# Kernel optimization log

Measured on AMD Instinct MI355X. Metric: run time of the kernel, lower is better.

The kernel has to match this reference:

```python
import jax, jax.numpy as jnp
import numpy as np

SEGMENT_LENGTHS = (2048, 4096, 8192)
DILATION_RATES = (1, 2, 4)
NUM_HEADS = 12
EMBED_DIM = 768
B, N = 2, 8192


def setup_inputs() -> dict:
    key = jax.random.key(0)
    ks = jax.random.split(key, 11)
    E = EMBED_DIM
    return {
        "query": jax.random.normal(ks[0], (B, N, E), jnp.float32),
        "key": jax.random.normal(ks[1], (B, N, E), jnp.float32),
        "value": jax.random.normal(ks[2], (B, N, E), jnp.float32),
        "Wq": jax.random.normal(ks[3], (E, E), jnp.float32) * (E ** -0.5),
        "bq": jax.random.normal(ks[4], (E,), jnp.float32) * 0.02,
        "Wk": jax.random.normal(ks[5], (E, E), jnp.float32) * (E ** -0.5),
        "bk": jax.random.normal(ks[6], (E,), jnp.float32) * 0.02,
        "Wv": jax.random.normal(ks[7], (E, E), jnp.float32) * (E ** -0.5),
        "bv": jax.random.normal(ks[8], (E,), jnp.float32) * 0.02,
        "Wo": jax.random.normal(ks[9], (E, E), jnp.float32) * (E ** -0.5),
        "bo": jax.random.normal(ks[10], (E,), jnp.float32) * 0.02,
    }


def _dilated_attention(q, k, v):
    # q, k, v: [b, n, h, d]
    b, n, h, d = q.shape
    num_groups = len(DILATION_RATES)
    g = h // num_groups  # heads per dilation group
    scale = float(1.0 / np.sqrt(d))  # xformers default softmax scale
    out = jnp.zeros_like(q)
    for i, (r, s) in enumerate(zip(DILATION_RATES, SEGMENT_LENGTHS)):
        off = i % r
        hmin, hmax = i * g, (i + 1) * g
        nseg = n // s
        # gather: [b, nseg, s/r, g, d]
        qg = q.reshape(b, nseg, s, h, d)[:, :, off::r, hmin:hmax, :]
        kg = k.reshape(b, nseg, s, h, d)[:, :, off::r, hmin:hmax, :]
        vg = v.reshape(b, nseg, s, h, d)[:, :, off::r, hmin:hmax, :]
        scores = jnp.einsum("bnqhd,bnkhd->bnhqk", qg, kg) * scale
        attn = jax.nn.softmax(scores, axis=-1)
        x = jnp.einsum("bnhqk,bnkhd->bnqhd", attn, vg)
        out = (
            out.reshape(b, nseg, s, h, d)
            .at[:, :, off::r, hmin:hmax, :]
            .add(x)
            .reshape(b, n, h, d)
        )
    # faithful to original: normalize by sum over the sequence dimension
    return out / jnp.sum(out, axis=1, keepdims=True)


def reference(query, key, value, Wq, bq, Wk, bk, Wv, bv, Wo, bo):
    b, n, e = query.shape
    h = NUM_HEADS
    d = e // h
    q = (query @ Wq.T + bq).reshape(b, n, h, d)
    k = (key @ Wk.T + bk).reshape(b, n, h, d)
    v = (value @ Wv.T + bv).reshape(b, n, h, d)
    x = _dilated_attention(q, k, v)
    x = x.reshape(b, n, e)
    return x @ Wo.T + bo
```

## Files before the change

kernel.cpp:

```cpp
#include <hip/hip_runtime.h>
#include <hip/hip_bf16.h>
#include <cmath>
#include <cstdint>

#define B_ 2
#define N_ 8192
#define H_ 12
#define D_ 64
#define E_ 768
#define M_ (B_*N_)

typedef __attribute__((ext_vector_type(8))) short short8;
typedef __attribute__((ext_vector_type(4))) short short4v;
typedef __attribute__((ext_vector_type(4))) float float4v;
typedef __attribute__((ext_vector_type(2))) unsigned uint2v;

__device__ inline short f2b(float f) {
  union { float f; unsigned u; } x; x.f = f;
  unsigned r = (x.u + 0x7fffu + ((x.u >> 16) & 1u)) >> 16;
  return (short)r;
}
__device__ inline float b2f(short s) {
  union { unsigned u; float f; } x; x.u = ((unsigned)(unsigned short)s) << 16;
  return x.f;
}
__device__ inline void split2(float f, short& h, short& l) {
  h = f2b(f);
  l = f2b(f - b2f(h));
}
__device__ inline void split_rn1(float f, unsigned& hi16, float& lo) {
  unsigned u = __float_as_uint(f);
  unsigned r = u + 0x7fffu + ((u >> 16) & 1u);
  hi16 = r >> 16;
  lo = f - __uint_as_float(hi16 << 16);
}
__device__ inline unsigned pack_trunc(float a, float b) {
  return (__float_as_uint(b) & 0xffff0000u) | (__float_as_uint(a) >> 16);
}

#define MFMA(a, b, c) __builtin_amdgcn_mfma_f32_16x16x32_bf16((a), (b), (c), 0, 0, 0)

#define GLOAD_LDS16(g, l) \
  __builtin_amdgcn_global_load_lds((const __attribute__((address_space(1))) void*)(g), \
      (__attribute__((address_space(3))) void*)(l), 16, 0, 0)

__global__ __launch_bounds__(256) void split_kernel(const float* __restrict__ src,
    short* __restrict__ hi, short* __restrict__ lo, int count4)
{
  int i = blockIdx.x * 256 + threadIdx.x;
  if (i >= count4) return;
  float4v t = ((const float4v*)src)[i];
  short4v h4, l4; short hh, ll;
  split2(t.x, hh, ll); h4.x = hh; l4.x = ll;
  split2(t.y, hh, ll); h4.y = hh; l4.y = ll;
  split2(t.z, hh, ll); h4.z = hh; l4.z = ll;
  split2(t.w, hh, ll); h4.w = hh; l4.w = ll;
  ((short4v*)hi)[i] = h4;
  ((short4v*)lo)[i] = l4;
}

__global__ __launch_bounds__(256) void inv_kernel(const float* __restrict__ sums,
    float* __restrict__ inv)
{
  int i = blockIdx.x * 256 + threadIdx.x;
  if (i < B_ * E_) inv[i] = 1.0f / sums[i];
}

template<int AMODE, bool OUT_PAIR>
__global__ __launch_bounds__(256) void gemm_xwT(const float* __restrict__ Ap,
    const float* __restrict__ inv, const short* __restrict__ Wh,
    const short* __restrict__ Wl, const float* __restrict__ bias,
    void* __restrict__ OutH, short* __restrict__ OutL)
{
  __shared__ short Ash[128 * 40], Asl[128 * 40];
  __shared__ short Wsh[128 * 32], Wsl[128 * 32];
  const int tid = threadIdx.x;
  const int m0 = blockIdx.y * 128;
  const int n0 = blockIdx.x * 128;
  const int w = tid >> 6, lane = tid & 63, quad = lane >> 4, l16 = lane & 15;
  const int wr = w >> 1, wc = w & 1;
  const int cq = (l16 >> 1) & 3;

  float4v acc[4][4];
#pragma unroll
  for (int a = 0; a < 4; ++a)
#pragma unroll
    for (int c = 0; c < 4; ++c) acc[a][c] = (float4v)0.0f;

  for (int kt = 0; kt < 24; ++kt) {
    const int k0 = kt * 32;
#pragma unroll
    for (int i = 0; i < 2; ++i) {
      int slot = w * 128 + i * 64 + lane;
      int row = slot >> 2, cs = slot & 3;
      int cl = cs ^ ((row >> 1) & 3);
      size_t go = (size_t)(n0 + row) * E_ + k0 + cl * 8;
      GLOAD_LDS16(Wh + go, &Wsh[slot * 8]);
      GLOAD_LDS16(Wl + go, &Wsl[slot * 8]);
    }
#pragma unroll
    for (int p = 0; p < 4; ++p) {
      int idx = tid + p * 256;
      int row = idx >> 3, c4 = (idx & 7) * 4;
      float4v t = *(const float4v*)(Ap + (size_t)(m0 + row) * E_ + k0 + c4);
      if constexpr (AMODE == 1) {
        float4v iv = *(const float4v*)(inv + (m0 >> 13) * E_ + k0 + c4);
        t *= iv;
      }
      unsigned h0, h1, h2, h3; float l0, l1, l2, l3;
      split_rn1(t.x, h0, l0); split_rn1(t.y, h1, l1);
      split_rn1(t.z, h2, l2); split_rn1(t.w, h3, l3);
      uint2v hp, lp;
      hp.x = h0 | (h1 << 16); hp.y = h2 | (h3 << 16);
      lp.x = pack_trunc(l0, l1); lp.y = pack_trunc(l2, l3);
      *(uint2v*)&Ash[row * 40 + c4] = hp;
      *(uint2v*)&Asl[row * 40 + c4] = lp;
    }
    __syncthreads();

    short8 afh[4], afl[4], bfh[4], bfl[4];
#pragma unroll
    for (int rt = 0; rt < 4; ++rt) {
      afh[rt] = *(const short8*)&Ash[(wr * 64 + rt * 16 + l16) * 40 + quad * 8];
      afl[rt] = *(const short8*)&Asl[(wr * 64 + rt * 16 + l16) * 40 + quad * 8];
    }
#pragma unroll
    for (int ct = 0; ct < 4; ++ct) {
      int wrow = (wc * 64 + ct * 16 + l16) * 32 + (quad ^ cq) * 8;
      bfh[ct] = *(const short8*)&Wsh[wrow];
      bfl[ct] = *(const short8*)&Wsl[wrow];
    }
#pragma unroll
    for (int rt = 0; rt < 4; ++rt)
#pragma unroll
      for (int ct = 0; ct < 4; ++ct) {
        float4v a = acc[rt][ct];
        a = MFMA(afh[rt], bfh[ct], a);
        a = MFMA(afh[rt], bfl[ct], a);
        a = MFMA(afl[rt], bfh[ct], a);
        acc[rt][ct] = a;
      }
    __syncthreads();
  }

#pragma unroll
  for (int ct = 0; ct < 4; ++ct) {
    int n = n0 + wc * 64 + ct * 16 + l16;
    float bv = bias[n];
#pragma unroll
    for (int rt = 0; rt < 4; ++rt) {
#pragma unroll
      for (int i = 0; i < 4; ++i) {
        int m = m0 + wr * 64 + rt * 16 + quad * 4 + i;
        float v = acc[rt][ct][i] + bv;
        if constexpr (OUT_PAIR) {
          short hh, ll; split2(v, hh, ll);
          ((short*)OutH)[(size_t)m * E_ + n] = hh;
          OutL[(size_t)m * E_ + n] = ll;
        } else {
          ((float*)OutH)[(size_t)m * E_ + n] = v;
        }
      }
    }
  }
}

__device__ __host__ inline int hoff_of(int g, int hg) {
  return g == 0 ? hg * 8192 : (g == 1 ? 32768 + hg * 4096 : 49152 + hg * 2048);
}

__global__ __launch_bounds__(256) void transpose_v(const short* __restrict__ vh,
    const short* __restrict__ vl, short* __restrict__ vgh, short* __restrict__ vgl)
{
  __shared__ short Lh[64 * 68], Ll[64 * 68];
  int bid = blockIdx.x;
  int b = 0;
  if (bid >= 896) { b = 1; bid -= 896; }
  int g, hg, tile;
  if (bid < 512)      { g = 0; hg = bid >> 7; tile = bid & 127; }
  else if (bid < 768) { g = 1; hg = (bid - 512) >> 6; tile = (bid - 512) & 63; }
  else                { g = 2; hg = (bid - 768) >> 5; tile = (bid - 768) & 31; }
  const int h = g * 4 + hg, r = 1 << g, off = g;
  const int ext = 8192 >> g;
  const int jj0 = tile * 64, seg = jj0 >> 11, j0 = jj0 & 2047;
  const int n0 = seg * (2048 << g) + off + j0 * r;
  const int tid = threadIdx.x;

#pragma unroll
  for (int p = 0; p < 2; ++p) {
    int c = tid + p * 256;
    int jr = c >> 3, c8 = (c & 7) * 8;
    size_t gsrc = ((size_t)(b * N_ + n0 + jr * r) * H_ + h) * D_ + c8;
    *(short8*)&Lh[jr * 68 + c8] = *(const short8*)(vh + gsrc);
    *(short8*)&Ll[jr * 68 + c8] = *(const short8*)(vl + gsrc);
  }
  __syncthreads();
  size_t basebh = ((size_t)b * 57344 + hoff_of(g, hg)) * 64;
#pragma unroll
  for (int p = 0; p < 2; ++p) {
    int c = tid + p * 256;
    int dd = c >> 3, jc = (c & 7) * 8;
    short8 oh, ol;
#pragma unroll
    for (int u = 0; u < 8; ++u) {
      oh[u] = Lh[(jc + u) * 68 + dd];
      ol[u] = Ll[(jc + u) * 68 + dd];
    }
    size_t gdst = basebh + (size_t)dd * ext + jj0 + jc;
    *(short8*)(vgh + gdst) = oh;
    *(short8*)(vgl + gdst) = ol;
  }
}

__global__ __launch_bounds__(256) void attn_kernel(
    const short* __restrict__ qh, const short* __restrict__ ql,
    const short* __restrict__ kh, const short* __restrict__ kl,
    const short* __restrict__ vgh, const short* __restrict__ vgl,
    float* __restrict__ attn_out, float* __restrict__ sums)
{
  __shared__ short Ksh[32 * 72], Ksl[32 * 72];
  __shared__ short Vth[64 * 40], Vtl[64 * 40];
  __shared__ short Psh[4][32 * 40], Psl[4][32 * 40];

  int bid = blockIdx.x;
  int g, t;
  if (bid < 512)      { g = 0; t = bid; }
  else if (bid < 768) { g = 1; t = bid - 512; }
  else                { g = 2; t = bid - 768; }
  const int qtile = t & 15; t >>= 4;
  const int hg = t & 3; t >>= 2;
  const int nseg = 4 >> g;
  const int seg = t & (nseg - 1);
  const int b = t / nseg;
  const int r = 1 << g;
  const int off = g;
  const int h = g * 4 + hg;
  const int segbase = seg * (2048 << g);
  const int ext = 8192 >> g;

  const int tid = threadIdx.x;
  const int w = tid >> 6, lane = tid & 63, quad = lane >> 4, l16 = lane & 15;

  const size_t vbase = ((size_t)b * 57344 + hoff_of(g, hg)) * 64 + (size_t)seg * 2048;

  if (g > 0) {
#pragma unroll
    for (int res0 = 1; res0 < 4; ++res0) {
      if (res0 >= r) break;
      int res = (off + res0) & (r - 1);
      for (int c = 0; c < 8; ++c) {
        int idx = tid + c * 256;
        int jl = idx >> 4, d0 = (idx & 15) * 4;
        int pos = segbase + res + (qtile * 128 + jl) * r;
        *(float4v*)(attn_out + ((size_t)(b * N_ + pos) * H_ + h) * D_ + d0) = (float4v)0.f;
      }
    }
  }

  short8 qfh[2][2], qfl[2][2];
#pragma unroll
  for (int qt = 0; qt < 2; ++qt) {
    int j = qtile * 128 + w * 32 + qt * 16 + l16;
    int pos = segbase + off + j * r;
    size_t base = ((size_t)(b * N_ + pos) * H_ + h) * D_;
#pragma unroll
    for (int ks = 0; ks < 2; ++ks) {
      qfh[qt][ks] = *(const short8*)(qh + base + ks * 32 + quad * 8);
      qfl[qt][ks] = *(const short8*)(ql + base + ks * 32 + quad * 8);
    }
  }

  float4v o[4][2];
  float mrow[2], lrow[2];
#pragma unroll
  for (int dt = 0; dt < 4; ++dt)
#pragma unroll
    for (int qt = 0; qt < 2; ++qt) o[dt][qt] = (float4v)0.0f;
  mrow[0] = mrow[1] = -INFINITY;
  lrow[0] = lrow[1] = 0.f;

  for (int kt = 0; kt < 64; ++kt) {
    {
      int row = tid >> 3, c8 = (tid & 7) * 8;
      int posk = segbase + off + (kt * 32 + row) * r;
      size_t gb = ((size_t)(b * N_ + posk) * H_ + h) * D_ + c8;
      *(short8*)&Ksh[row * 72 + c8] = *(const short8*)(kh + gb);
      *(short8*)&Ksl[row * 72 + c8] = *(const short8*)(kl + gb);
      int dd = tid >> 2, kvc = (tid & 3) * 8;
      size_t vb = vbase + (size_t)dd * ext + kt * 32 + kvc;
      *(short8*)&Vth[dd * 40 + kvc] = *(const short8*)(vgh + vb);
      *(short8*)&Vtl[dd * 40 + kvc] = *(const short8*)(vgl + vb);
    }
    __syncthreads();

    float4v sc[2][2];
#pragma unroll
    for (int kvt = 0; kvt < 2; ++kvt) {
      const int kb = (kvt * 16 + l16) * 72 + quad * 8;
      short8 ah0 = *(const short8*)&Ksh[kb];
      short8 ah1 = *(const short8*)&Ksh[kb + 32];
      short8 al0 = *(const short8*)&Ksl[kb];
      short8 al1 = *(const short8*)&Ksl[kb + 32];
#pragma unroll
      for (int qt = 0; qt < 2; ++qt) {
        float4v a = (float4v)0.0f;
        a = MFMA(ah0, qfh[qt][0], a); a = MFMA(ah1, qfh[qt][1], a);
        a = MFMA(ah0, qfl[qt][0], a); a = MFMA(ah1, qfl[qt][1], a);
        a = MFMA(al0, qfh[qt][0], a); a = MFMA(al1, qfh[qt][1], a);
        sc[qt][kvt] = a * 0.125f;
      }
    }

#pragma unroll
    for (int qt = 0; qt < 2; ++qt) {
      float mx = sc[qt][0][0];
#pragma unroll
      for (int kvt = 0; kvt < 2; ++kvt)
#pragma unroll
        for (int i = 0; i < 4; ++i) mx = fmaxf(mx, sc[qt][kvt][i]);
      mx = fmaxf(mx, __shfl_xor(mx, 16, 64));
      mx = fmaxf(mx, __shfl_xor(mx, 32, 64));
      if (__any(mx > mrow[qt])) {
        float mnew = fmaxf(mrow[qt], mx);
        float alpha = __expf(mrow[qt] - mnew);
        mrow[qt] = mnew;
        lrow[qt] *= alpha;
#pragma unroll
        for (int dt = 0; dt < 4; ++dt) o[dt][qt] *= alpha;
      }
      float rs = 0.f;
#pragma unroll
      for (int kvt = 0; kvt < 2; ++kvt)
#pragma unroll
        for (int i = 0; i < 4; ++i) {
          float p = __expf(sc[qt][kvt][i] - mrow[qt]);
          sc[qt][kvt][i] = p;
          rs += p;
        }
      rs += __shfl_xor(rs, 16, 64);
      rs += __shfl_xor(rs, 32, 64);
      lrow[qt] += rs;

#pragma unroll
      for (int kvt = 0; kvt < 2; ++kvt)
#pragma unroll
        for (int c = 0; c < 2; ++c) {
          float pa = sc[qt][kvt][2 * c], pb = sc[qt][kvt][2 * c + 1];
          unsigned ua = __float_as_uint(pa), ub = __float_as_uint(pb);
          float la = pa - __uint_as_float(ua & 0xffff0000u);
          float lb = pb - __uint_as_float(ub & 0xffff0000u);
          int ad = (qt * 16 + l16) * 40 + kvt * 16 + quad * 4 + 2 * c;
          *(unsigned*)&Psh[w][ad] = (ub & 0xffff0000u) | (ua >> 16);
          *(unsigned*)&Psl[w][ad] = pack_trunc(la, lb);
        }
    }

    short8 pfh[2], pfl[2];
#pragma unroll
    for (int qt = 0; qt < 2; ++qt) {
      pfh[qt] = *(const short8*)&Psh[w][(qt * 16 + l16) * 40 + quad * 8];
      pfl[qt] = *(const short8*)&Psl[w][(qt * 16 + l16) * 40 + quad * 8];
    }
#pragma unroll
    for (int dt = 0; dt < 4; ++dt) {
      short8 vfh = *(const short8*)&Vth[(dt * 16 + l16) * 40 + quad * 8];
      short8 vfl = *(const short8*)&Vtl[(dt * 16 + l16) * 40 + quad * 8];
#pragma unroll
      for (int qt = 0; qt < 2; ++qt) {
        float4v a = o[dt][qt];
        a = MFMA(vfh, pfh[qt], a);
        a = MFMA(vfh, pfl[qt], a);
        a = MFMA(vfl, pfh[qt], a);
        o[dt][qt] = a;
      }
    }
    __syncthreads();
  }

  float4v sacc[4];
#pragma unroll
  for (int dt = 0; dt < 4; ++dt) sacc[dt] = (float4v)0.0f;
#pragma unroll
  for (int qt = 0; qt < 2; ++qt) {
    float inv_l = 1.0f / lrow[qt];
    int j = qtile * 128 + w * 32 + qt * 16 + l16;
    int pos = segbase + off + j * r;
    float* dst = attn_out + ((size_t)(b * N_ + pos) * H_ + h) * D_;
#pragma unroll
    for (int dt = 0; dt < 4; ++dt) {
      float4v v = o[dt][qt] * inv_l;
      *(float4v*)(dst + dt * 16 + quad * 4) = v;
      sacc[dt] += v;
    }
  }
#pragma unroll
  for (int dt = 0; dt < 4; ++dt) {
#pragma unroll
    for (int i = 0; i < 4; ++i) {
      float x = sacc[dt][i];
      x += __shfl_xor(x, 1, 64);
      x += __shfl_xor(x, 2, 64);
      x += __shfl_xor(x, 4, 64);
      x += __shfl_xor(x, 8, 64);
      if (l16 == 0)
        atomicAdd(&sums[(size_t)b * E_ + h * D_ + dt * 16 + quad * 4 + i], x);
    }
  }
}

extern "C" void kernel_launch(void* const* d_in, const int* in_sizes, int n_in,
                              void* d_out, int out_size, void* d_ws, size_t ws_size,
                              hipStream_t stream)
{
  const float* query = (const float*)d_in[0];
  const float* key_  = (const float*)d_in[1];
  const float* value = (const float*)d_in[2];
  const float* Wq = (const float*)d_in[3];
  const float* bq = (const float*)d_in[4];
  const float* Wk = (const float*)d_in[5];
  const float* bk = (const float*)d_in[6];
  const float* Wv = (const float*)d_in[7];
  const float* bv = (const float*)d_in[8];
  const float* Wo = (const float*)d_in[9];
  const float* bo = (const float*)d_in[10];

  char* ws = (char*)d_ws;
  const size_t szbf = (size_t)M_ * E_ * 2;
  const size_t szvg = (size_t)2 * 57344 * 64 * 2;
  const size_t szw  = (size_t)E_ * E_ * 2;
  short* qh_ = (short*)(ws);
  short* ql_ = (short*)(ws + 1 * szbf);
  short* kh_ = (short*)(ws + 2 * szbf);
  short* kl_ = (short*)(ws + 3 * szbf);
  short* vh_ = (short*)(ws + 4 * szbf);
  short* vl_ = (short*)(ws + 5 * szbf);
  short* vgh = (short*)(ws + 6 * szbf);
  short* vgl = (short*)(ws + 6 * szbf + szvg);
  short* wsp = (short*)(ws + 6 * szbf + 2 * szvg);
  short* wqh = wsp + 0 * (szw / 2), *wql = wsp + 1 * (szw / 2);
  short* wkh = wsp + 2 * (szw / 2), *wkl = wsp + 3 * (szw / 2);
  short* wvh = wsp + 4 * (szw / 2), *wvl = wsp + 5 * (szw / 2);
  short* woh = wsp + 6 * (szw / 2), *wol = wsp + 7 * (szw / 2);
  float* sums = (float*)(ws + 6 * szbf + 2 * szvg + 8 * szw);
  float* attn = (float*)(ws + 4 * szbf);
  float* inv  = (float*)qh_;

  hipMemsetAsync(sums, 0, (size_t)B_ * E_ * sizeof(float), stream);

  const int wc4 = E_ * E_ / 4;
  split_kernel<<<(wc4 + 255) / 256, 256, 0, stream>>>(Wq, wqh, wql, wc4);
  split_kernel<<<(wc4 + 255) / 256, 256, 0, stream>>>(Wk, wkh, wkl, wc4);
  split_kernel<<<(wc4 + 255) / 256, 256, 0, stream>>>(Wv, wvh, wvl, wc4);
  split_kernel<<<(wc4 + 255) / 256, 256, 0, stream>>>(Wo, woh, wol, wc4);

  dim3 gg(6, 128), gb(256);
  gemm_xwT<0, true><<<gg, gb, 0, stream>>>(query, nullptr, wqh, wql, bq, qh_, ql_);
  gemm_xwT<0, true><<<gg, gb, 0, stream>>>(key_,  nullptr, wkh, wkl, bk, kh_, kl_);
  gemm_xwT<0, true><<<gg, gb, 0, stream>>>(value, nullptr, wvh, wvl, bv, vh_, vl_);
  transpose_v<<<1792, 256, 0, stream>>>(vh_, vl_, vgh, vgl);
  attn_kernel<<<896, 256, 0, stream>>>(qh_, ql_, kh_, kl_, vgh, vgl, attn, sums);
  inv_kernel<<<6, 256, 0, stream>>>(sums, inv);
  gemm_xwT<1, false><<<gg, gb, 0, stream>>>(attn, inv, woh, wol, bo, d_out, nullptr);
}
```

Before: 886.5 us.

## Pre-split GEMM activations to bf16 hi/lo planes and DMA both operands into LDS

Adds separate kernels that split the fp32 activations into bf16 hi/lo planes before each projection GEMM. A prep kernel also applies the output normalisation before the final projection. The GEMM then loads both A and W tiles with direct global-to-LDS loads and a swizzled layout, dropping the in-loop fp32 load, split and LDS store work. The four weight-split launches are merged into one. This trades extra global traffic (writing and re-reading bf16 planes) and extra launches for a simpler, more DMA-friendly GEMM inner loop.

```diff
diff --git a/kernel.cpp b/kernel.cpp
--- a/kernel.cpp
+++ b/kernel.cpp
@@ -13,7 +13,6 @@
 typedef __attribute__((ext_vector_type(8))) short short8;
 typedef __attribute__((ext_vector_type(4))) short short4v;
 typedef __attribute__((ext_vector_type(4))) float float4v;
-typedef __attribute__((ext_vector_type(2))) unsigned uint2v;
 
 __device__ inline short f2b(float f) {
   union { float f; unsigned u; } x; x.f = f;
@@ -27,12 +26,6 @@
 __device__ inline void split2(float f, short& h, short& l) {
   h = f2b(f);
   l = f2b(f - b2f(h));
-}
-__device__ inline void split_rn1(float f, unsigned& hi16, float& lo) {
-  unsigned u = __float_as_uint(f);
-  unsigned r = u + 0x7fffu + ((u >> 16) & 1u);
-  hi16 = r >> 16;
-  lo = f - __uint_as_float(hi16 << 16);
 }
 __device__ inline unsigned pack_trunc(float a, float b) {
   return (__float_as_uint(b) & 0xffff0000u) | (__float_as_uint(a) >> 16);
@@ -59,6 +52,27 @@
   ((short4v*)lo)[i] = l4;
 }
 
+__global__ __launch_bounds__(256) void split_w4(
+    const float* __restrict__ w0, const float* __restrict__ w1,
+    const float* __restrict__ w2, const float* __restrict__ w3,
+    short* __restrict__ planes)
+{
+  int which = blockIdx.y;
+  const float* src = which == 0 ? w0 : which == 1 ? w1 : which == 2 ? w2 : w3;
+  short* hi = planes + (size_t)(2 * which) * (E_ * E_);
+  short* lo = planes + (size_t)(2 * which + 1) * (E_ * E_);
+  int i = blockIdx.x * 256 + threadIdx.x;
+  if (i >= E_ * E_ / 4) return;
+  float4v t = ((const float4v*)src)[i];
+  short4v h4, l4; short hh, ll;
+  split2(t.x, hh, ll); h4.x = hh; l4.x = ll;
+  split2(t.y, hh, ll); h4.y = hh; l4.y = ll;
+  split2(t.z, hh, ll); h4.z = hh; l4.z = ll;
+  split2(t.w, hh, ll); h4.w = hh; l4.w = ll;
+  ((short4v*)hi)[i] = h4;
+  ((short4v*)lo)[i] = l4;
+}
+
 __global__ __launch_bounds__(256) void inv_kernel(const float* __restrict__ sums,
     float* __restrict__ inv)
 {
@@ -66,20 +80,39 @@
   if (i < B_ * E_) inv[i] = 1.0f / sums[i];
 }
 
-template<int AMODE, bool OUT_PAIR>
-__global__ __launch_bounds__(256) void gemm_xwT(const float* __restrict__ Ap,
-    const float* __restrict__ inv, const short* __restrict__ Wh,
-    const short* __restrict__ Wl, const float* __restrict__ bias,
-    void* __restrict__ OutH, short* __restrict__ OutL)
-{
-  __shared__ short Ash[128 * 40], Asl[128 * 40];
-  __shared__ short Wsh[128 * 32], Wsl[128 * 32];
+__global__ __launch_bounds__(256) void prep_out(const float* __restrict__ attn,
+    const float* __restrict__ inv, short* __restrict__ xnh, short* __restrict__ xnl)
+{
+  size_t e4 = ((size_t)blockIdx.x * 256 + threadIdx.x) * 4;
+  int e = (int)(e4 % E_);
+  int b = (int)(e4 / ((size_t)E_ * N_));
+  float4v a = *(const float4v*)(attn + e4);
+  float4v iv = *(const float4v*)(inv + (size_t)b * E_ + e);
+  a *= iv;
+  short4v h4, l4; short hh, ll;
+  split2(a.x, hh, ll); h4.x = hh; l4.x = ll;
+  split2(a.y, hh, ll); h4.y = hh; l4.y = ll;
+  split2(a.z, hh, ll); h4.z = hh; l4.z = ll;
+  split2(a.w, hh, ll); h4.w = hh; l4.w = ll;
+  *(short4v*)&xnh[e4] = h4;
+  *(short4v*)&xnl[e4] = l4;
+}
+
+template<bool OUT_PAIR>
+__global__ __launch_bounds__(256) void gemm_dma(
+    const short* __restrict__ Ah, const short* __restrict__ Al,
+    const short* __restrict__ Wh, const short* __restrict__ Wl,
+    const float* __restrict__ bias, void* __restrict__ OutH, short* __restrict__ OutL)
+{
+  __shared__ short Ash[4096], Asl[4096], Wsh[4096], Wsl[4096];
   const int tid = threadIdx.x;
   const int m0 = blockIdx.y * 128;
   const int n0 = blockIdx.x * 128;
   const int w = tid >> 6, lane = tid & 63, quad = lane >> 4, l16 = lane & 15;
   const int wr = w >> 1, wc = w & 1;
   const int cq = (l16 >> 1) & 3;
+  const int dmarow = lane >> 2;
+  const int dmacc = (((lane & 3) ^ ((lane >> 3) & 3))) * 8;
 
   float4v acc[4][4];
 #pragma unroll
@@ -91,44 +124,26 @@
     const int k0 = kt * 32;
 #pragma unroll
     for (int i = 0; i < 2; ++i) {
-      int slot = w * 128 + i * 64 + lane;
-      int row = slot >> 2, cs = slot & 3;
-      int cl = cs ^ ((row >> 1) & 3);
-      size_t go = (size_t)(n0 + row) * E_ + k0 + cl * 8;
-      GLOAD_LDS16(Wh + go, &Wsh[slot * 8]);
-      GLOAD_LDS16(Wl + go, &Wsl[slot * 8]);
-    }
-#pragma unroll
-    for (int p = 0; p < 4; ++p) {
-      int idx = tid + p * 256;
-      int row = idx >> 3, c4 = (idx & 7) * 4;
-      float4v t = *(const float4v*)(Ap + (size_t)(m0 + row) * E_ + k0 + c4);
-      if constexpr (AMODE == 1) {
-        float4v iv = *(const float4v*)(inv + (m0 >> 13) * E_ + k0 + c4);
-        t *= iv;
-      }
-      unsigned h0, h1, h2, h3; float l0, l1, l2, l3;
-      split_rn1(t.x, h0, l0); split_rn1(t.y, h1, l1);
-      split_rn1(t.z, h2, l2); split_rn1(t.w, h3, l3);
-      uint2v hp, lp;
-      hp.x = h0 | (h1 << 16); hp.y = h2 | (h3 << 16);
-      lp.x = pack_trunc(l0, l1); lp.y = pack_trunc(l2, l3);
-      *(uint2v*)&Ash[row * 40 + c4] = hp;
-      *(uint2v*)&Asl[row * 40 + c4] = lp;
+      int c = w * 2 + i;
+      int ldso = c * 512 + lane * 8;
+      size_t ga = (size_t)(m0 + c * 16 + dmarow) * E_ + k0 + dmacc;
+      size_t gw = (size_t)(n0 + c * 16 + dmarow) * E_ + k0 + dmacc;
+      GLOAD_LDS16(Ah + ga, &Ash[ldso]);
+      GLOAD_LDS16(Al + ga, &Asl[ldso]);
+      GLOAD_LDS16(Wh + gw, &Wsh[ldso]);
+      GLOAD_LDS16(Wl + gw, &Wsl[ldso]);
     }
     __syncthreads();
 
     short8 afh[4], afl[4], bfh[4], bfl[4];
 #pragma unroll
     for (int rt = 0; rt < 4; ++rt) {
-      afh[rt] = *(const short8*)&Ash[(wr * 64 + rt * 16 + l16) * 40 + quad * 8];
-      afl[rt] = *(const short8*)&Asl[(wr * 64 + rt * 16 + l16) * 40 + quad * 8];
-    }
-#pragma unroll
-    for (int ct = 0; ct < 4; ++ct) {
-      int wrow = (wc * 64 + ct * 16 + l16) * 32 + (quad ^ cq) * 8;
-      bfh[ct] = *(const short8*)&Wsh[wrow];
-      bfl[ct] = *(const short8*)&Wsl[wrow];
+      int ao = (wr * 64 + rt * 16 + l16) * 32 + (quad ^ cq) * 8;
+      afh[rt] = *(const short8*)&Ash[ao];
+      afl[rt] = *(const short8*)&Asl[ao];
+      int wo = (wc * 64 + rt * 16 + l16) * 32 + (quad ^ cq) * 8;
+      bfh[rt] = *(const short8*)&Wsh[wo];
+      bfl[rt] = *(const short8*)&Wsl[wo];
     }
 #pragma unroll
     for (int rt = 0; rt < 4; ++rt)
@@ -434,31 +449,37 @@
   short* kl_ = (short*)(ws + 3 * szbf);
   short* vh_ = (short*)(ws + 4 * szbf);
   short* vl_ = (short*)(ws + 5 * szbf);
+  short* ish = (short*)(ws + 6 * szbf);
+  short* isl = (short*)(ws + 7 * szbf);
   short* vgh = (short*)(ws + 6 * szbf);
   short* vgl = (short*)(ws + 6 * szbf + szvg);
-  short* wsp = (short*)(ws + 6 * szbf + 2 * szvg);
+  short* wsp = (short*)(ws + 8 * szbf);
+  float* sums = (float*)(ws + 8 * szbf + 8 * szw);
+  float* attn = (float*)(ws + 4 * szbf);
+  float* inv  = (float*)qh_;
+  short* xnh = kh_;
+  short* xnl = kl_;
   short* wqh = wsp + 0 * (szw / 2), *wql = wsp + 1 * (szw / 2);
   short* wkh = wsp + 2 * (szw / 2), *wkl = wsp + 3 * (szw / 2);
   short* wvh = wsp + 4 * (szw / 2), *wvl = wsp + 5 * (szw / 2);
   short* woh = wsp + 6 * (szw / 2), *wol = wsp + 7 * (szw / 2);
-  float* sums = (float*)(ws + 6 * szbf + 2 * szvg + 8 * szw);
-  float* attn = (float*)(ws + 4 * szbf);
-  float* inv  = (float*)qh_;
 
   hipMemsetAsync(sums, 0, (size_t)B_ * E_ * sizeof(float), stream);
 
-  const int wc4 = E_ * E_ / 4;
-  split_kernel<<<(wc4 + 255) / 256, 256, 0, stream>>>(Wq, wqh, wql, wc4);
-  split_kernel<<<(wc4 + 255) / 256, 256, 0, stream>>>(Wk, wkh, wkl, wc4);
-  split_kernel<<<(wc4 + 255) / 256, 256, 0, stream>>>(Wv, wvh, wvl, wc4);
-  split_kernel<<<(wc4 + 255) / 256, 256, 0, stream>>>(Wo, woh, wol, wc4);
-
+  split_w4<<<dim3(576, 4), 256, 0, stream>>>(Wq, Wk, Wv, Wo, wsp);
+
+  const int ac4 = M_ * E_ / 4;
   dim3 gg(6, 128), gb(256);
-  gemm_xwT<0, true><<<gg, gb, 0, stream>>>(query, nullptr, wqh, wql, bq, qh_, ql_);
-  gemm_xwT<0, true><<<gg, gb, 0, stream>>>(key_,  nullptr, wkh, wkl, bk, kh_, kl_);
-  gemm_xwT<0, true><<<gg, gb, 0, stream>>>(value, nullptr, wvh, wvl, bv, vh_, vl_);
+  split_kernel<<<12288, 256, 0, stream>>>(query, ish, isl, ac4);
+  gemm_dma<true><<<gg, gb, 0, stream>>>(ish, isl, wqh, wql, bq, qh_, ql_);
+  split_kernel<<<12288, 256, 0, stream>>>(key_, ish, isl, ac4);
+  gemm_dma<true><<<gg, gb, 0, stream>>>(ish, isl, wkh, wkl, bk, kh_, kl_);
+  split_kernel<<<12288, 256, 0, stream>>>(value, ish, isl, ac4);
+  gemm_dma<true><<<gg, gb, 0, stream>>>(ish, isl, wvh, wvl, bv, vh_, vl_);
+
   transpose_v<<<1792, 256, 0, stream>>>(vh_, vl_, vgh, vgl);
   attn_kernel<<<896, 256, 0, stream>>>(qh_, ql_, kh_, kl_, vgh, vgl, attn, sums);
   inv_kernel<<<6, 256, 0, stream>>>(sums, inv);
-  gemm_xwT<1, false><<<gg, gb, 0, stream>>>(attn, inv, woh, wol, bo, d_out, nullptr);
-}
+  prep_out<<<12288, 256, 0, stream>>>(attn, inv, xnh, xnl);
+  gemm_dma<false><<<gg, gb, 0, stream>>>(xnh, xnl, woh, wol, bo, d_out, nullptr);
+}
```

After: 877.3 us. Within noise of the previous version (-1.0%).
